# Kernel optimization log

Measured on AMD Instinct MI355X. Metric: run time of the kernel, lower is better.

## Reference

```python
import jax, jax.numpy as jnp
import numpy as np

D_MODEL = 1024
N_HEADS = 16
NUM_EXPERTS = 8
GATE_HIDDEN = 128
B, T = 4, 2048


def setup_inputs() -> dict:
    key = jax.random.key(0)
    ks = jax.random.split(key, 14)
    s = 0.02
    d, e, gh = D_MODEL, NUM_EXPERTS, GATE_HIDDEN
    return {
        "hidden_states": jax.random.normal(ks[0], (B, T, d), jnp.float32),
        # torch Linear weights are [out_features, in_features]
        "Wq": jax.random.normal(ks[1], (e, d, d), jnp.float32) * s,
        "bq": jax.random.normal(ks[2], (e, d), jnp.float32) * s,
        "Wk": jax.random.normal(ks[3], (e, d, d), jnp.float32) * s,
        "bk": jax.random.normal(ks[4], (e, d), jnp.float32) * s,
        "Wv": jax.random.normal(ks[5], (e, d, d), jnp.float32) * s,
        "bv": jax.random.normal(ks[6], (e, d), jnp.float32) * s,
        "Wg1": jax.random.normal(ks[7], (gh, d), jnp.float32) * s,
        "bg1": jax.random.normal(ks[8], (gh,), jnp.float32) * s,
        "Wg2": jax.random.normal(ks[9], (e, gh), jnp.float32) * s,
        "bg2": jax.random.normal(ks[10], (e,), jnp.float32) * s,
        "Wo": jax.random.normal(ks[11], (d, d), jnp.float32) * s,
        "bo": jax.random.normal(ks[12], (d,), jnp.float32) * s,
    }


def reference(hidden_states, Wq, bq, Wk, bk, Wv, bv, Wg1, bg1, Wg2, bg2, Wo, bo):
    Bb, Tt, C = hidden_states.shape
    H = N_HEADS
    Dh = C // H

    # Per-sample gating over mean-pooled sequence
    pooled = hidden_states.mean(axis=1)                        # [B, C]
    gate_h = jax.nn.relu(pooled @ Wg1.T + bg1)                 # [B, 128]
    gw = jax.nn.softmax(gate_h @ Wg2.T + bg2, axis=-1)         # [B, E]

    # Since gating weights are per-batch scalars, sum_e w_e * (x W_e^T + b_e)
    # == x (sum_e w_e W_e)^T + sum_e w_e b_e  — same math, one GEMM per sample.
    def proj(We, be):
        W_eff = jnp.einsum('be,eoi->boi', gw, We)              # [B, C, C]
        b_eff = gw @ be                                        # [B, C]
        y = jnp.einsum('bti,boi->bto', hidden_states, W_eff) + b_eff[:, None, :]
        return y.reshape(Bb, Tt, H, Dh).transpose(0, 2, 1, 3)  # [B, H, T, Dh]

    q = proj(Wq, bq)
    k = proj(Wk, bk)
    v = proj(Wv, bv)

    scores = jnp.einsum('bhtd,bhsd->bhts', q, k) / (Dh ** 0.5)
    attn = jax.nn.softmax(scores, axis=-1)                     # dropout is inference identity
    out = jnp.einsum('bhts,bhsd->bhtd', attn, v)
    out = out.transpose(0, 2, 1, 3).reshape(Bb, Tt, C)
    return out @ Wo.T + bo
```

## Files before the change

### kernel.cpp

```cpp
#include <hip/hip_runtime.h>

#define B_ 4
#define T_ 2048
#define C_ 1024
#define H_ 16
#define DH_ 64
#define E_ 8
#define GH_ 128

typedef unsigned short bf16_t;
typedef __attribute__((ext_vector_type(8))) __bf16 bf16x8;
typedef __attribute__((ext_vector_type(2))) __bf16 bf16x2;
typedef __attribute__((ext_vector_type(4))) float floatx4;
typedef __attribute__((ext_vector_type(16))) float floatx16;

#if __has_builtin(__builtin_amdgcn_exp2f)
#define EXP2F(x) __builtin_amdgcn_exp2f(x)
#else
#define EXP2F(x) exp2f(x)
#endif

__device__ __forceinline__ bf16_t f2bf(float f) {
  unsigned int u = __builtin_bit_cast(unsigned int, f);
  u += 0x7fffu + ((u >> 16) & 1u);
  return (bf16_t)(u >> 16);
}
__device__ __forceinline__ void async16(const void* g, void* l) {
  __builtin_amdgcn_global_load_lds(
      (const __attribute__((address_space(1))) unsigned int*)g,
      (__attribute__((address_space(3))) unsigned int*)l, 16, 0, 0);
}

__global__ void cvt_kernel(const float* __restrict__ src, bf16_t* __restrict__ dst) {
  int i = (blockIdx.x * 256 + threadIdx.x) * 4;
  float4 v = *(const float4*)(src + i);
  bf16_t o4[4] = {f2bf(v.x), f2bf(v.y), f2bf(v.z), f2bf(v.w)};
  *(uint2*)(dst + i) = *(const uint2*)o4;
}

__global__ void pool_kernel(const float* __restrict__ x, float* __restrict__ partial) {
  int bz = blockIdx.x;
  int b = bz >> 4;
  int r0 = (bz & 15) * 128;
  int t = threadIdx.x;
  float a0 = 0.f, a1 = 0.f, a2 = 0.f, a3 = 0.f;
  const float* xb = x + (size_t)b * T_ * C_ + (size_t)r0 * C_;
  for (int r = 0; r < 128; ++r) {
    const float* row = xb + (size_t)r * C_;
    a0 += row[t]; a1 += row[t + 256]; a2 += row[t + 512]; a3 += row[t + 768];
  }
  float* p = partial + (size_t)bz * C_;
  p[t] = a0; p[t + 256] = a1; p[t + 512] = a2; p[t + 768] = a3;
}

__global__ void gate_kernel(const float* __restrict__ partial,
                            const float* __restrict__ Wg1, const float* __restrict__ bg1,
                            const float* __restrict__ Wg2, const float* __restrict__ bg2,
                            const float* __restrict__ bq, const float* __restrict__ bk,
                            const float* __restrict__ bv,
                            float* __restrict__ gw, float* __restrict__ beff) {
  int b = blockIdx.x;
  int t = threadIdx.x;
  __shared__ float spool[C_];
  __shared__ float sh[GH_];
  __shared__ float sgw[E_];
  for (int i = t; i < C_; i += GH_) {
    float s = 0.f;
    for (int j = 0; j < 16; ++j) s += partial[(size_t)(b * 16 + j) * C_ + i];
    spool[i] = s * (1.0f / T_);
  }
  __syncthreads();
  {
    float acc = 0.f;
    const float* wr = Wg1 + (size_t)t * C_;
    for (int i = 0; i < C_; i += 4) {
      float4 w = *(const float4*)(wr + i);
      acc += spool[i] * w.x + spool[i + 1] * w.y + spool[i + 2] * w.z + spool[i + 3] * w.w;
    }
    acc += bg1[t];
    sh[t] = fmaxf(acc, 0.0f);
  }
  __syncthreads();
  if (t < E_) {
    float acc = 0.f;
    const float* wr = Wg2 + t * GH_;
    for (int j = 0; j < GH_; ++j) acc += sh[j] * wr[j];
    sgw[t] = acc + bg2[t];
  }
  __syncthreads();
  if (t == 0) {
    float mx = sgw[0];
    for (int e = 1; e < E_; ++e) mx = fmaxf(mx, sgw[e]);
    float s = 0.f, ex[E_];
    for (int e = 0; e < E_; ++e) { ex[e] = __expf(sgw[e] - mx); s += ex[e]; }
    float inv = 1.0f / s;
    for (int e = 0; e < E_; ++e) { sgw[e] = ex[e] * inv; gw[b * E_ + e] = sgw[e]; }
  }
  __syncthreads();
  for (int o = t; o < C_; o += GH_) {
    float aq = 0.f, ak = 0.f, av = 0.f;
    #pragma unroll
    for (int e = 0; e < E_; ++e) {
      float w = sgw[e];
      aq += w * bq[e * C_ + o];
      ak += w * bk[e * C_ + o];
      av += w * bv[e * C_ + o];
    }
    beff[(0 * B_ + b) * C_ + o] = aq;
    beff[(1 * B_ + b) * C_ + o] = ak;
    beff[(2 * B_ + b) * C_ + o] = av;
  }
}

__global__ void combine_kernel(const float* __restrict__ Wq, const float* __restrict__ Wk,
                               const float* __restrict__ Wv, const float* __restrict__ gw,
                               bf16_t* __restrict__ Weff) {
  int g = blockIdx.x * 256 + threadIdx.x;
  int ig = (g & 127) * 8;
  int o = (g >> 7) & 1023;
  int p = g >> 17;
  const float* W = (p == 0) ? Wq : (p == 1) ? Wk : Wv;
  const float* src = W + (size_t)o * C_ + ig;
  float acc[B_][8];
  #pragma unroll
  for (int b = 0; b < B_; ++b)
    #pragma unroll
    for (int j = 0; j < 8; ++j) acc[b][j] = 0.f;
  #pragma unroll
  for (int e = 0; e < E_; ++e) {
    float4 lo = *(const float4*)(src + (size_t)e * C_ * C_);
    float4 hi = *(const float4*)(src + (size_t)e * C_ * C_ + 4);
    float w8[8] = {lo.x, lo.y, lo.z, lo.w, hi.x, hi.y, hi.z, hi.w};
    #pragma unroll
    for (int b = 0; b < B_; ++b) {
      float wgt = gw[b * E_ + e];
      #pragma unroll
      for (int j = 0; j < 8; ++j) acc[b][j] += wgt * w8[j];
    }
  }
  #pragma unroll
  for (int b = 0; b < B_; ++b) {
    bf16_t out8[8];
    #pragma unroll
    for (int j = 0; j < 8; ++j) out8[j] = f2bf(acc[b][j]);
    *(uint4*)(Weff + ((size_t)p * B_ + b) * C_ * C_ + (size_t)o * C_ + ig) = *(const uint4*)out8;
  }
}

template <int MODE>
__global__ __launch_bounds__(256) void gemm128(const bf16_t* __restrict__ X,
                                               const bf16_t* __restrict__ W,
                                               const float* __restrict__ bias,
                                               bf16_t* __restrict__ Yb,
                                               float* __restrict__ Yf) {
  int n0, m0;
  if (MODE == 0) {
    const int L = blockIdx.x;
    const int wid = (L & 7) * 192 + (L >> 3);
    const int b = wid / 384;
    const int r = wid - b * 384;
    const int p = r >> 7;
    const int r2 = r & 127;
    const int z = p * 4 + b;
    n0 = (r2 & 7) * 128;
    m0 = (r2 >> 3) * 128;
    X += (size_t)b * (T_ * C_);
    W += (size_t)z * (C_ * C_);
    bias += (size_t)z * C_;
    Yb += (size_t)z * (T_ * C_);
  } else {
    const int L = blockIdx.x;
    const int wid = (L & 7) * 64 + (L >> 3);
    n0 = (wid & 7) * 128;
    m0 = (wid >> 3) * 128;
  }

  __shared__ __align__(16) bf16_t As[128][64];
  __shared__ __align__(16) bf16_t Bs[128][64];

  const int tid = threadIdx.x;
  const int wave = tid >> 6;
  const int lane = tid & 63;
  const int quad = lane >> 4;
  const int l16 = lane & 15;
  const int wm = (wave & 1) * 64;
  const int wn = (wave >> 1) * 64;

  floatx4 acc[4][4];
  #pragma unroll
  for (int i = 0; i < 4; ++i)
    #pragma unroll
    for (int j = 0; j < 4; ++j) { floatx4 zz = {0.f, 0.f, 0.f, 0.f}; acc[i][j] = zz; }

  const int ar = tid >> 3;
  const int ac = (tid & 7) * 8;
  const int sc = ((tid & 7) ^ (ar & 7)) * 8;
  const bf16_t* Xp = X + (size_t)(m0 + ar) * C_ + sc;
  const bf16_t* Wp = W + (size_t)(n0 + ar) * C_ + sc;

  const int x7 = l16 & 7;

  for (int k0 = 0; k0 < C_; k0 += 64) {
    __syncthreads();
    #pragma unroll
    for (int s = 0; s < 4; ++s) {
      async16(Xp + (size_t)(s * 32) * C_ + k0, &As[ar + s * 32][ac]);
      async16(Wp + (size_t)(s * 32) * C_ + k0, &Bs[ar + s * 32][ac]);
    }
    __syncthreads();
    #pragma unroll
    for (int kk = 0; kk < 64; kk += 32) {
      const int cofs = (((kk >> 3) + quad) ^ x7) * 8;
      bf16x8 af[4], bfr[4];
      #pragma unroll
      for (int i = 0; i < 4; ++i) {
        af[i] = *(const bf16x8*)(&As[wm + i * 16 + l16][cofs]);
        bfr[i] = *(const bf16x8*)(&Bs[wn + i * 16 + l16][cofs]);
      }
      #pragma unroll
      for (int mi = 0; mi < 4; ++mi)
        #pragma unroll
        for (int ni = 0; ni < 4; ++ni)
          acc[mi][ni] = __builtin_amdgcn_mfma_f32_16x16x32_bf16(af[mi], bfr[ni], acc[mi][ni], 0, 0, 0);
    }
  }

  #pragma unroll
  for (int mi = 0; mi < 4; ++mi) {
    #pragma unroll
    for (int ni = 0; ni < 4; ++ni) {
      const int n = n0 + wn + ni * 16 + l16;
      const float bv = bias[n];
      #pragma unroll
      for (int r = 0; r < 4; ++r) {
        const int m = m0 + wm + mi * 16 + quad * 4 + r;
        float v = acc[mi][ni][r] + bv;
        if (MODE == 0) Yb[((size_t)(n >> 6) * T_ + m) * DH_ + (n & 63)] = f2bf(v);
        else           Yf[(size_t)m * C_ + n] = v;
      }
    }
  }
}

__global__ void vtrans_kernel(const bf16_t* __restrict__ qkv, bf16_t* __restrict__ Vt) {
  const int kt = blockIdx.x;
  const int bh = blockIdx.y;
  const int b = bh >> 4, h = bh & 15;
  const bf16_t* src = qkv + (size_t)(8 + b) * T_ * C_ + (size_t)h * T_ * DH_ + (size_t)kt * 64 * DH_;
  __shared__ __align__(16) bf16_t L[64][64];
  const int t = threadIdx.x;
  const int r = t >> 2;
  const int c = (t & 3) * 16;
  const int sw = r & 48;
  *(uint4*)(&L[r][c ^ sw]) = *(const uint4*)(src + (size_t)r * DH_ + c);
  *(uint4*)(&L[r][(c ^ sw) + 8]) = *(const uint4*)(src + (size_t)r * DH_ + c + 8);
  __syncthreads();
  const int sw2 = c & 48;
  bf16_t tmp[16];
  #pragma unroll
  for (int j = 0; j < 16; ++j) tmp[j] = L[c + j][r ^ sw2];
  bf16_t* dst = Vt + (size_t)bh * DH_ * T_ + (size_t)r * T_ + (size_t)kt * 64 + c;
  *(uint4*)(dst) = *(const uint4*)(tmp);
  *(uint4*)(dst + 8) = *(const uint4*)(tmp + 8);
}

__global__ __launch_bounds__(512, 4) void attn_kernel(const bf16_t* __restrict__ qkv,
                                                      const bf16_t* __restrict__ Vt,
                                                      bf16_t* __restrict__ out) {
  const int bh = blockIdx.x;
  const int qt = blockIdx.y;
  const int b = bh >> 4, h = bh & 15;
  const __bf16* Q = (const __bf16*)(qkv + (size_t)b * T_ * C_ + (size_t)h * T_ * DH_);
  const bf16_t* Kp = qkv + (size_t)(4 + b) * T_ * C_ + (size_t)h * T_ * DH_;
  const bf16_t* Vtb = Vt + (size_t)bh * DH_ * T_;

  __shared__ __align__(16) bf16_t Ks[2][4096];
  __shared__ __align__(16) bf16_t Vs[2][4096];

  const int tid = threadIdx.x;
  const int wave = tid >> 6;
  const int lane = tid & 63;
  const int l31 = lane & 31;
  const int half = lane >> 5;

  const float QSC = 0.125f * 1.44269504f;
  bf16x8 qb[4];
  {
    const __bf16* qrow = Q + (size_t)(qt * 256 + wave * 32 + l31) * DH_;
    #pragma unroll
    for (int kc = 0; kc < 4; ++kc) {
      union { bf16x8 v; __bf16 e[8]; } fr;
      #pragma unroll
      for (int j = 0; j < 8; ++j) fr.e[j] = (__bf16)((float)qrow[kc * 16 + half * 8 + j] * QSC);
      qb[kc] = fr.v;
    }
  }

  int koff[2][4];
  int voff[4][2];
  #pragma unroll
  for (int kb = 0; kb < 2; ++kb)
    #pragma unroll
    for (int kc = 0; kc < 4; ++kc) {
      int r = kb * 32 + l31;
      koff[kb][kc] = (r * 8 + ((kc * 2 + half) ^ (r & 7))) * 8;
    }
  #pragma unroll
  for (int c = 0; c < 4; ++c)
    #pragma unroll
    for (int db = 0; db < 2; ++db) {
      int r = db * 32 + l31;
      voff[c][db] = (r * 8 + ((c * 2 + half) ^ (r & 7))) * 8;
    }

  floatx16 oacc[2];
  #pragma unroll
  for (int db = 0; db < 2; ++db)
    #pragma unroll
    for (int i = 0; i < 16; ++i) oacc[db][i] = 0.f;
  float lrun = 0.f;

  const int srow = tid >> 3;
  const int schk = (tid & 7) ^ (srow & 7);
  const bf16_t* kg = Kp + (size_t)srow * DH_ + schk * 8;
  const bf16_t* vg = Vtb + (size_t)srow * T_ + schk * 8;

#define STAGE(BUF) do {                                   \
    async16(kg, &Ks[BUF][tid * 8]);                       \
    async16(vg, &Vs[BUF][tid * 8]);                       \
    kg += 64 * DH_;                                       \
    vg += 64;                                             \
  } while (0)

#define WAITV(N) asm volatile("s_waitcnt vmcnt(" #N ")" ::: "memory")
#define BAR() __builtin_amdgcn_s_barrier()

#define COMPUTE(CUR) do {                                                            \
    _Pragma("unroll")                                                                \
    for (int kb = 0; kb < 2; ++kb) {                                                 \
      floatx16 s_;                                                                   \
      _Pragma("unroll")                                                              \
      for (int i = 0; i < 16; ++i) s_[i] = 0.f;                                      \
      __builtin_amdgcn_s_setprio(1);                                                 \
      _Pragma("unroll")                                                              \
      for (int kc = 0; kc < 4; ++kc) {                                               \
        bf16x8 ka = *(const bf16x8*)(&Ks[CUR][koff[kb][kc]]);                        \
        s_ = __builtin_amdgcn_mfma_f32_32x32x16_bf16(ka, qb[kc], s_, 0, 0, 0);       \
      }                                                                              \
      __builtin_amdgcn_s_setprio(0);                                                 \
      _Pragma("unroll")                                                              \
      for (int cl = 0; cl < 2; ++cl) {                                               \
        float e0 = EXP2F(s_[cl * 8 + 0]);                                            \
        float e1 = EXP2F(s_[cl * 8 + 1]);                                            \
        float e2 = EXP2F(s_[cl * 8 + 2]);                                            \
        float e3 = EXP2F(s_[cl * 8 + 3]);                                            \
        float e4 = EXP2F(s_[cl * 8 + 4]);                                            \
        float e5 = EXP2F(s_[cl * 8 + 5]);                                            \
        float e6 = EXP2F(s_[cl * 8 + 6]);                                            \
        float e7 = EXP2F(s_[cl * 8 + 7]);                                            \
        lrun += ((e0 + e1) + (e2 + e3)) + ((e4 + e5) + (e6 + e7));                   \
        bf16x2 w01 = {(__bf16)e0, (__bf16)e1};                                       \
        bf16x2 w23 = {(__bf16)e2, (__bf16)e3};                                       \
        bf16x2 w45 = {(__bf16)e4, (__bf16)e5};                                       \
        bf16x2 w67 = {(__bf16)e6, (__bf16)e7};                                       \
        unsigned int ua = __builtin_bit_cast(unsigned int, w01);                     \
        unsigned int ub = __builtin_bit_cast(unsigned int, w23);                     \
        unsigned int uc = __builtin_bit_cast(unsigned int, w45);                     \
        unsigned int ud = __builtin_bit_cast(unsigned int, w67);                     \
        asm("v_permlane32_swap_b32 %0, %1" : "+v"(ua), "+v"(uc));                    \
        asm("v_permlane32_swap_b32 %0, %1" : "+v"(ub), "+v"(ud));                    \
        union { unsigned int u[4]; bf16x8 v; } pf;                                   \
        pf.u[0] = ua; pf.u[1] = ub; pf.u[2] = uc; pf.u[3] = ud;                      \
        __builtin_amdgcn_s_setprio(1);                                               \
        _Pragma("unroll")                                                            \
        for (int db = 0; db < 2; ++db) {                                             \
          bf16x8 vb = *(const bf16x8*)(&Vs[CUR][voff[kb * 2 + cl][db]]);             \
          oacc[db] = __builtin_amdgcn_mfma_f32_32x32x16_bf16(pf.v, vb, oacc[db], 0, 0, 0); \
        }                                                                            \
        __builtin_amdgcn_s_setprio(0);                                               \
      }                                                                              \
    }                                                                                \
  } while (0)

  STAGE(0);
  #pragma unroll 1
  for (int kt = 0; kt < 30; kt += 2) {
    STAGE(1);
    WAITV(2);
    BAR();
    COMPUTE(0);
    BAR();
    STAGE(0);
    WAITV(2);
    BAR();
    COMPUTE(1);
    BAR();
  }
  STAGE(1);
  WAITV(2);
  BAR();
  COMPUTE(0);
  BAR();
  WAITV(0);
  BAR();
  COMPUTE(1);

#undef STAGE
#undef WAITV
#undef BAR
#undef COMPUTE

  lrun += __shfl_xor(lrun, 32);
  float linv = 1.0f / lrun;
  #pragma unroll
  for (int reg = 0; reg < 16; ++reg) {
    int mr = (reg & 3) + 8 * (reg >> 2) + 4 * half;
    float li = __shfl(linv, (lane & 32) | mr);
    int m = qt * 256 + wave * 32 + mr;
    #pragma unroll
    for (int db = 0; db < 2; ++db) {
      out[(size_t)b * T_ * C_ + (size_t)m * C_ + h * DH_ + db * 32 + l31] =
          f2bf(oacc[db][reg] * li);
    }
  }
}

extern "C" void kernel_launch(void* const* d_in, const int* in_sizes, int n_in,
                              void* d_out, int out_size, void* d_ws, size_t ws_size,
                              hipStream_t stream) {
  (void)in_sizes; (void)n_in; (void)out_size; (void)ws_size;
  const float* x   = (const float*)d_in[0];
  const float* Wq  = (const float*)d_in[1];
  const float* bq  = (const float*)d_in[2];
  const float* Wk  = (const float*)d_in[3];
  const float* bk  = (const float*)d_in[4];
  const float* Wv  = (const float*)d_in[5];
  const float* bv  = (const float*)d_in[6];
  const float* Wg1 = (const float*)d_in[7];
  const float* bg1 = (const float*)d_in[8];
  const float* Wg2 = (const float*)d_in[9];
  const float* bg2 = (const float*)d_in[10];
  const float* Wo  = (const float*)d_in[11];
  const float* bo  = (const float*)d_in[12];

  char* ws = (char*)d_ws;
  size_t off = 0;
  auto alloc = [&](size_t bytes) -> void* {
    void* p = ws + off;
    off += (bytes + 255) & ~(size_t)255;
    return p;
  };
  float* partial = (float*)alloc((size_t)B_ * 16 * C_ * 4);
  float* gw      = (float*)alloc((size_t)B_ * E_ * 4);
  float* beff    = (float*)alloc((size_t)3 * B_ * C_ * 4);
  bf16_t* xbf    = (bf16_t*)alloc((size_t)B_ * T_ * C_ * 2);
  bf16_t* Wobf   = (bf16_t*)alloc((size_t)C_ * C_ * 2);
  bf16_t* Weff   = (bf16_t*)alloc((size_t)3 * B_ * C_ * C_ * 2);
  bf16_t* qkv    = (bf16_t*)alloc((size_t)3 * B_ * T_ * C_ * 2);
  bf16_t* attn   = (bf16_t*)alloc((size_t)B_ * T_ * C_ * 2);
  bf16_t* Vt = xbf;

  pool_kernel<<<dim3(B_ * 16), 256, 0, stream>>>(x, partial);
  gate_kernel<<<dim3(B_), GH_, 0, stream>>>(partial, Wg1, bg1, Wg2, bg2,
                                            bq, bk, bv, gw, beff);
  combine_kernel<<<dim3(3 * C_ * (C_ / 8) / 256), 256, 0, stream>>>(Wq, Wk, Wv, gw, Weff);
  cvt_kernel<<<dim3((B_ * T_ * C_) / 1024), 256, 0, stream>>>(x, xbf);
  cvt_kernel<<<dim3((C_ * C_) / 1024), 256, 0, stream>>>(Wo, Wobf);
  gemm128<0><<<dim3(12 * (T_ / 128) * (C_ / 128)), 256, 0, stream>>>(xbf, Weff, beff, qkv, nullptr);
  vtrans_kernel<<<dim3(T_ / 64, B_ * H_), 256, 0, stream>>>(qkv, Vt);
  attn_kernel<<<dim3(B_ * H_, T_ / 256), 512, 0, stream>>>(qkv, Vt, attn);
  gemm128<1><<<dim3(((B_ * T_) / 128) * (C_ / 128)), 256, 0, stream>>>(attn, Wobf, bo, nullptr, (float*)d_out);
}
```

Measured before the change: 411.1 us.

## Fuse x bf16 conversion into pooling; shrink attention blocks to 256 threads

The pooling kernel now also writes the bf16 copy of the hidden states. This removes the separate conversion pass and a second full read of x. It uses 256 blocks of 32 rows with float4 loads, and the gate kernel sums 64 partials instead of 16. The attention kernel moves from 512-thread blocks covering 256 queries to 256-thread blocks covering 128 queries, doubling the grid. Each thread now issues two async loads each for K and V per stage, so the wait counts are adjusted and the V offsets reuse the K offset table.

```diff
diff --git a/kernel.cpp b/kernel.cpp
--- a/kernel.cpp
+++ b/kernel.cpp
@@ -38,19 +38,22 @@
   *(uint2*)(dst + i) = *(const uint2*)o4;
 }
 
-__global__ void pool_kernel(const float* __restrict__ x, float* __restrict__ partial) {
-  int bz = blockIdx.x;
-  int b = bz >> 4;
-  int r0 = (bz & 15) * 128;
-  int t = threadIdx.x;
-  float a0 = 0.f, a1 = 0.f, a2 = 0.f, a3 = 0.f;
-  const float* xb = x + (size_t)b * T_ * C_ + (size_t)r0 * C_;
-  for (int r = 0; r < 128; ++r) {
-    const float* row = xb + (size_t)r * C_;
-    a0 += row[t]; a1 += row[t + 256]; a2 += row[t + 512]; a3 += row[t + 768];
-  }
-  float* p = partial + (size_t)bz * C_;
-  p[t] = a0; p[t + 256] = a1; p[t + 512] = a2; p[t + 768] = a3;
+__global__ void pool_kernel(const float* __restrict__ x, float* __restrict__ partial,
+                            bf16_t* __restrict__ xbf) {
+  const int bz = blockIdx.x;
+  const int b = bz >> 6;
+  const int r0 = (bz & 63) * 32;
+  const int t = threadIdx.x;
+  float4 acc = {0.f, 0.f, 0.f, 0.f};
+  const float* xb = x + (size_t)b * T_ * C_ + (size_t)r0 * C_ + t * 4;
+  bf16_t* ob = xbf + (size_t)b * T_ * C_ + (size_t)r0 * C_ + t * 4;
+  for (int r = 0; r < 32; ++r) {
+    float4 v = *(const float4*)(xb + (size_t)r * C_);
+    acc.x += v.x; acc.y += v.y; acc.z += v.z; acc.w += v.w;
+    bf16_t o4[4] = {f2bf(v.x), f2bf(v.y), f2bf(v.z), f2bf(v.w)};
+    *(uint2*)(ob + (size_t)r * C_) = *(const uint2*)o4;
+  }
+  *(float4*)(partial + (size_t)bz * C_ + t * 4) = acc;
 }
 
 __global__ void gate_kernel(const float* __restrict__ partial,
@@ -66,7 +69,7 @@
   __shared__ float sgw[E_];
   for (int i = t; i < C_; i += GH_) {
     float s = 0.f;
-    for (int j = 0; j < 16; ++j) s += partial[(size_t)(b * 16 + j) * C_ + i];
+    for (int j = 0; j < 64; ++j) s += partial[(size_t)(b * 64 + j) * C_ + i];
     spool[i] = s * (1.0f / T_);
   }
   __syncthreads();
@@ -264,7 +267,7 @@
   *(uint4*)(dst + 8) = *(const uint4*)(tmp + 8);
 }
 
-__global__ __launch_bounds__(512, 4) void attn_kernel(const bf16_t* __restrict__ qkv,
+__global__ __launch_bounds__(256, 4) void attn_kernel(const bf16_t* __restrict__ qkv,
                                                       const bf16_t* __restrict__ Vt,
                                                       bf16_t* __restrict__ out) {
   const int bh = blockIdx.x;
@@ -286,7 +289,7 @@
   const float QSC = 0.125f * 1.44269504f;
   bf16x8 qb[4];
   {
-    const __bf16* qrow = Q + (size_t)(qt * 256 + wave * 32 + l31) * DH_;
+    const __bf16* qrow = Q + (size_t)(qt * 128 + wave * 32 + l31) * DH_;
     #pragma unroll
     for (int kc = 0; kc < 4; ++kc) {
       union { bf16x8 v; __bf16 e[8]; } fr;
@@ -297,20 +300,12 @@
   }
 
   int koff[2][4];
-  int voff[4][2];
   #pragma unroll
   for (int kb = 0; kb < 2; ++kb)
     #pragma unroll
     for (int kc = 0; kc < 4; ++kc) {
       int r = kb * 32 + l31;
       koff[kb][kc] = (r * 8 + ((kc * 2 + half) ^ (r & 7))) * 8;
-    }
-  #pragma unroll
-  for (int c = 0; c < 4; ++c)
-    #pragma unroll
-    for (int db = 0; db < 2; ++db) {
-      int r = db * 32 + l31;
-      voff[c][db] = (r * 8 + ((c * 2 + half) ^ (r & 7))) * 8;
     }
 
   floatx16 oacc[2];
@@ -325,11 +320,13 @@
   const bf16_t* kg = Kp + (size_t)srow * DH_ + schk * 8;
   const bf16_t* vg = Vtb + (size_t)srow * T_ + schk * 8;
 
-#define STAGE(BUF) do {                                   \
-    async16(kg, &Ks[BUF][tid * 8]);                       \
-    async16(vg, &Vs[BUF][tid * 8]);                       \
-    kg += 64 * DH_;                                       \
-    vg += 64;                                             \
+#define STAGE(BUF) do {                                           \
+    async16(kg, &Ks[BUF][tid * 8]);                               \
+    async16(kg + 32 * DH_, &Ks[BUF][2048 + tid * 8]);             \
+    async16(vg, &Vs[BUF][tid * 8]);                               \
+    async16(vg + (size_t)32 * T_, &Vs[BUF][2048 + tid * 8]);      \
+    kg += 64 * DH_;                                               \
+    vg += 64;                                                     \
   } while (0)
 
 #define WAITV(N) asm volatile("s_waitcnt vmcnt(" #N ")" ::: "memory")
@@ -374,7 +371,7 @@
         __builtin_amdgcn_s_setprio(1);                                               \
         _Pragma("unroll")                                                            \
         for (int db = 0; db < 2; ++db) {                                             \
-          bf16x8 vb = *(const bf16x8*)(&Vs[CUR][voff[kb * 2 + cl][db]]);             \
+          bf16x8 vb = *(const bf16x8*)(&Vs[CUR][koff[db][kb * 2 + cl]]);             \
           oacc[db] = __builtin_amdgcn_mfma_f32_32x32x16_bf16(pf.v, vb, oacc[db], 0, 0, 0); \
         }                                                                            \
         __builtin_amdgcn_s_setprio(0);                                               \
@@ -386,18 +383,18 @@
   #pragma unroll 1
   for (int kt = 0; kt < 30; kt += 2) {
     STAGE(1);
-    WAITV(2);
+    WAITV(4);
     BAR();
     COMPUTE(0);
     BAR();
     STAGE(0);
-    WAITV(2);
+    WAITV(4);
     BAR();
     COMPUTE(1);
     BAR();
   }
   STAGE(1);
-  WAITV(2);
+  WAITV(4);
   BAR();
   COMPUTE(0);
   BAR();
@@ -416,7 +413,7 @@
   for (int reg = 0; reg < 16; ++reg) {
     int mr = (reg & 3) + 8 * (reg >> 2) + 4 * half;
     float li = __shfl(linv, (lane & 32) | mr);
-    int m = qt * 256 + wave * 32 + mr;
+    int m = qt * 128 + wave * 32 + mr;
     #pragma unroll
     for (int db = 0; db < 2; ++db) {
       out[(size_t)b * T_ * C_ + (size_t)m * C_ + h * DH_ + db * 32 + l31] =
@@ -450,7 +447,7 @@
     off += (bytes + 255) & ~(size_t)255;
     return p;
   };
-  float* partial = (float*)alloc((size_t)B_ * 16 * C_ * 4);
+  float* partial = (float*)alloc((size_t)B_ * 64 * C_ * 4);
   float* gw      = (float*)alloc((size_t)B_ * E_ * 4);
   float* beff    = (float*)alloc((size_t)3 * B_ * C_ * 4);
   bf16_t* xbf    = (bf16_t*)alloc((size_t)B_ * T_ * C_ * 2);
@@ -460,14 +457,13 @@
   bf16_t* attn   = (bf16_t*)alloc((size_t)B_ * T_ * C_ * 2);
   bf16_t* Vt = xbf;
 
-  pool_kernel<<<dim3(B_ * 16), 256, 0, stream>>>(x, partial);
+  pool_kernel<<<dim3(B_ * 64), 256, 0, stream>>>(x, partial, xbf);
   gate_kernel<<<dim3(B_), GH_, 0, stream>>>(partial, Wg1, bg1, Wg2, bg2,
                                             bq, bk, bv, gw, beff);
   combine_kernel<<<dim3(3 * C_ * (C_ / 8) / 256), 256, 0, stream>>>(Wq, Wk, Wv, gw, Weff);
-  cvt_kernel<<<dim3((B_ * T_ * C_) / 1024), 256, 0, stream>>>(x, xbf);
   cvt_kernel<<<dim3((C_ * C_) / 1024), 256, 0, stream>>>(Wo, Wobf);
   gemm128<0><<<dim3(12 * (T_ / 128) * (C_ / 128)), 256, 0, stream>>>(xbf, Weff, beff, qkv, nullptr);
   vtrans_kernel<<<dim3(T_ / 64, B_ * H_), 256, 0, stream>>>(qkv, Vt);
-  attn_kernel<<<dim3(B_ * H_, T_ / 256), 512, 0, stream>>>(qkv, Vt, attn);
+  attn_kernel<<<dim3(B_ * H_, T_ / 128), 256, 0, stream>>>(qkv, Vt, attn);
   gemm128<1><<<dim3(((B_ * T_) / 128) * (C_ / 128)), 256, 0, stream>>>(attn, Wobf, bo, nullptr, (float*)d_out);
 }
```

Result: no change. 409.0 us (-0.5%).

## Fuse x bf16 conversion into pooling, bias mixing and V transpose into QKV GEMM

Applied to the files above, without the earlier changes.

The pooling kernel now also writes the bf16 copy of the input, so the separate conversion pass over x is gone and x is read once. The effective bias mixing moves from the gate kernel into the QKV GEMM epilogue, which forms it from the gating weights. The V projection is written directly in transposed [d][t] layout through an LDS-staged, swizzled epilogue, which removes the separate vtrans kernel and its extra read and write of V. In exchange the GEMM epilogue does more work and the pooling uses four times as many partial sums.

```diff
diff --git a/kernel.cpp b/kernel.cpp
--- a/kernel.cpp
+++ b/kernel.cpp
@@ -38,27 +38,28 @@
   *(uint2*)(dst + i) = *(const uint2*)o4;
 }
 
-__global__ void pool_kernel(const float* __restrict__ x, float* __restrict__ partial) {
-  int bz = blockIdx.x;
-  int b = bz >> 4;
-  int r0 = (bz & 15) * 128;
-  int t = threadIdx.x;
-  float a0 = 0.f, a1 = 0.f, a2 = 0.f, a3 = 0.f;
-  const float* xb = x + (size_t)b * T_ * C_ + (size_t)r0 * C_;
-  for (int r = 0; r < 128; ++r) {
-    const float* row = xb + (size_t)r * C_;
-    a0 += row[t]; a1 += row[t + 256]; a2 += row[t + 512]; a3 += row[t + 768];
-  }
-  float* p = partial + (size_t)bz * C_;
-  p[t] = a0; p[t + 256] = a1; p[t + 512] = a2; p[t + 768] = a3;
+__global__ void pool_kernel(const float* __restrict__ x, float* __restrict__ partial,
+                            bf16_t* __restrict__ xbf) {
+  const int bz = blockIdx.x;
+  const int b = bz >> 6;
+  const int r0 = (bz & 63) * 32;
+  const int t = threadIdx.x;
+  float4 acc = {0.f, 0.f, 0.f, 0.f};
+  const float* xb = x + (size_t)b * T_ * C_ + (size_t)r0 * C_ + t * 4;
+  bf16_t* ob = xbf + (size_t)b * T_ * C_ + (size_t)r0 * C_ + t * 4;
+  for (int r = 0; r < 32; ++r) {
+    float4 v = *(const float4*)(xb + (size_t)r * C_);
+    acc.x += v.x; acc.y += v.y; acc.z += v.z; acc.w += v.w;
+    bf16_t o4[4] = {f2bf(v.x), f2bf(v.y), f2bf(v.z), f2bf(v.w)};
+    *(uint2*)(ob + (size_t)r * C_) = *(const uint2*)o4;
+  }
+  *(float4*)(partial + (size_t)bz * C_ + t * 4) = acc;
 }
 
 __global__ void gate_kernel(const float* __restrict__ partial,
                             const float* __restrict__ Wg1, const float* __restrict__ bg1,
                             const float* __restrict__ Wg2, const float* __restrict__ bg2,
-                            const float* __restrict__ bq, const float* __restrict__ bk,
-                            const float* __restrict__ bv,
-                            float* __restrict__ gw, float* __restrict__ beff) {
+                            float* __restrict__ gw) {
   int b = blockIdx.x;
   int t = threadIdx.x;
   __shared__ float spool[C_];
@@ -66,7 +67,7 @@
   __shared__ float sgw[E_];
   for (int i = t; i < C_; i += GH_) {
     float s = 0.f;
-    for (int j = 0; j < 16; ++j) s += partial[(size_t)(b * 16 + j) * C_ + i];
+    for (int j = 0; j < 64; ++j) s += partial[(size_t)(b * 64 + j) * C_ + i];
     spool[i] = s * (1.0f / T_);
   }
   __syncthreads();
@@ -94,21 +95,7 @@
     float s = 0.f, ex[E_];
     for (int e = 0; e < E_; ++e) { ex[e] = __expf(sgw[e] - mx); s += ex[e]; }
     float inv = 1.0f / s;
-    for (int e = 0; e < E_; ++e) { sgw[e] = ex[e] * inv; gw[b * E_ + e] = sgw[e]; }
-  }
-  __syncthreads();
-  for (int o = t; o < C_; o += GH_) {
-    float aq = 0.f, ak = 0.f, av = 0.f;
-    #pragma unroll
-    for (int e = 0; e < E_; ++e) {
-      float w = sgw[e];
-      aq += w * bq[e * C_ + o];
-      ak += w * bk[e * C_ + o];
-      av += w * bv[e * C_ + o];
-    }
-    beff[(0 * B_ + b) * C_ + o] = aq;
-    beff[(1 * B_ + b) * C_ + o] = ak;
-    beff[(2 * B_ + b) * C_ + o] = av;
+    for (int e = 0; e < E_; ++e) gw[b * E_ + e] = ex[e] * inv;
   }
 }
 
@@ -151,9 +138,15 @@
 __global__ __launch_bounds__(256) void gemm128(const bf16_t* __restrict__ X,
                                                const bf16_t* __restrict__ W,
                                                const float* __restrict__ bias,
+                                               const float* __restrict__ bq,
+                                               const float* __restrict__ bk,
+                                               const float* __restrict__ bv,
+                                               const float* __restrict__ gw,
                                                bf16_t* __restrict__ Yb,
                                                float* __restrict__ Yf) {
   int n0, m0;
+  int pp = 0, bb = 0;
+  const float* bsrc = nullptr;
   if (MODE == 0) {
     const int L = blockIdx.x;
     const int wid = (L & 7) * 192 + (L >> 3);
@@ -166,8 +159,9 @@
     m0 = (r2 >> 3) * 128;
     X += (size_t)b * (T_ * C_);
     W += (size_t)z * (C_ * C_);
-    bias += (size_t)z * C_;
     Yb += (size_t)z * (T_ * C_);
+    pp = p; bb = b;
+    bsrc = (p == 0) ? bq : (p == 1) ? bk : bv;
   } else {
     const int L = blockIdx.x;
     const int wid = (L & 7) * 64 + (L >> 3);
@@ -175,8 +169,9 @@
     m0 = (wid >> 3) * 128;
   }
 
-  __shared__ __align__(16) bf16_t As[128][64];
-  __shared__ __align__(16) bf16_t Bs[128][64];
+  __shared__ __align__(16) bf16_t smem[2][128][64];
+  bf16_t (*As)[64] = smem[0];
+  bf16_t (*Bs)[64] = smem[1];
 
   const int tid = threadIdx.x;
   const int wave = tid >> 6;
@@ -186,6 +181,12 @@
   const int wm = (wave & 1) * 64;
   const int wn = (wave >> 1) * 64;
 
+  float gwv[E_];
+  if (MODE == 0) {
+    #pragma unroll
+    for (int e = 0; e < E_; ++e) gwv[e] = gw[bb * E_ + e];
+  }
+
   floatx4 acc[4][4];
   #pragma unroll
   for (int i = 0; i < 4; ++i)
@@ -225,16 +226,63 @@
     }
   }
 
+  float be_[4];
+  #pragma unroll
+  for (int ni = 0; ni < 4; ++ni) {
+    const int n = n0 + wn + ni * 16 + l16;
+    if (MODE == 0) {
+      float s = 0.f;
+      #pragma unroll
+      for (int e = 0; e < E_; ++e) s += gwv[e] * bsrc[(size_t)e * C_ + n];
+      be_[ni] = s;
+    } else {
+      be_[ni] = bias[n];
+    }
+  }
+
+  if (MODE == 0 && pp == 2) {
+    __syncthreads();
+    bf16_t* Ls = &smem[0][0][0];
+    #pragma unroll
+    for (int ni = 0; ni < 4; ++ni) {
+      const int n = wn + ni * 16 + l16;
+      #pragma unroll
+      for (int mi = 0; mi < 4; ++mi) {
+        const int mb = wm + mi * 16 + quad * 4;
+        bf16_t o4[4];
+        #pragma unroll
+        for (int r = 0; r < 4; ++r) o4[r] = f2bf(acc[mi][ni][r] + be_[ni]);
+        const int c = mb >> 3;
+        const int csw = (c & 8) | ((c ^ n) & 7);
+        *(uint2*)((char*)(Ls + (size_t)n * 128) + csw * 16 + (mb & 7) * 2) =
+            *(const uint2*)o4;
+      }
+    }
+    __syncthreads();
+    const int n = tid >> 1;
+    const int mh = (tid & 1) * 64;
+    const int head = (n0 + n) >> 6;
+    const int d = (n0 + n) & 63;
+    bf16_t* dst = Yb + (size_t)head * (DH_ * T_) + (size_t)d * T_ + m0 + mh;
+    #pragma unroll
+    for (int j = 0; j < 8; ++j) {
+      const int c = (mh >> 3) + j;
+      const int csw = (c & 8) | ((c ^ n) & 7);
+      *(uint4*)(dst + j * 8) =
+          *(const uint4*)((const char*)(Ls + (size_t)n * 128) + csw * 16);
+    }
+    return;
+  }
+
   #pragma unroll
   for (int mi = 0; mi < 4; ++mi) {
     #pragma unroll
     for (int ni = 0; ni < 4; ++ni) {
       const int n = n0 + wn + ni * 16 + l16;
-      const float bv = bias[n];
       #pragma unroll
       for (int r = 0; r < 4; ++r) {
         const int m = m0 + wm + mi * 16 + quad * 4 + r;
-        float v = acc[mi][ni][r] + bv;
+        float v = acc[mi][ni][r] + be_[ni];
         if (MODE == 0) Yb[((size_t)(n >> 6) * T_ + m) * DH_ + (n & 63)] = f2bf(v);
         else           Yf[(size_t)m * C_ + n] = v;
       }
@@ -242,37 +290,14 @@
   }
 }
 
-__global__ void vtrans_kernel(const bf16_t* __restrict__ qkv, bf16_t* __restrict__ Vt) {
-  const int kt = blockIdx.x;
-  const int bh = blockIdx.y;
-  const int b = bh >> 4, h = bh & 15;
-  const bf16_t* src = qkv + (size_t)(8 + b) * T_ * C_ + (size_t)h * T_ * DH_ + (size_t)kt * 64 * DH_;
-  __shared__ __align__(16) bf16_t L[64][64];
-  const int t = threadIdx.x;
-  const int r = t >> 2;
-  const int c = (t & 3) * 16;
-  const int sw = r & 48;
-  *(uint4*)(&L[r][c ^ sw]) = *(const uint4*)(src + (size_t)r * DH_ + c);
-  *(uint4*)(&L[r][(c ^ sw) + 8]) = *(const uint4*)(src + (size_t)r * DH_ + c + 8);
-  __syncthreads();
-  const int sw2 = c & 48;
-  bf16_t tmp[16];
-  #pragma unroll
-  for (int j = 0; j < 16; ++j) tmp[j] = L[c + j][r ^ sw2];
-  bf16_t* dst = Vt + (size_t)bh * DH_ * T_ + (size_t)r * T_ + (size_t)kt * 64 + c;
-  *(uint4*)(dst) = *(const uint4*)(tmp);
-  *(uint4*)(dst + 8) = *(const uint4*)(tmp + 8);
-}
-
 __global__ __launch_bounds__(512, 4) void attn_kernel(const bf16_t* __restrict__ qkv,
-                                                      const bf16_t* __restrict__ Vt,
                                                       bf16_t* __restrict__ out) {
   const int bh = blockIdx.x;
   const int qt = blockIdx.y;
   const int b = bh >> 4, h = bh & 15;
   const __bf16* Q = (const __bf16*)(qkv + (size_t)b * T_ * C_ + (size_t)h * T_ * DH_);
   const bf16_t* Kp = qkv + (size_t)(4 + b) * T_ * C_ + (size_t)h * T_ * DH_;
-  const bf16_t* Vtb = Vt + (size_t)bh * DH_ * T_;
+  const bf16_t* Vtb = qkv + (size_t)(8 + b) * T_ * C_ + (size_t)h * DH_ * T_;
 
   __shared__ __align__(16) bf16_t Ks[2][4096];
   __shared__ __align__(16) bf16_t Vs[2][4096];
@@ -450,24 +475,21 @@
     off += (bytes + 255) & ~(size_t)255;
     return p;
   };
-  float* partial = (float*)alloc((size_t)B_ * 16 * C_ * 4);
+  float* partial = (float*)alloc((size_t)B_ * 64 * C_ * 4);
   float* gw      = (float*)alloc((size_t)B_ * E_ * 4);
-  float* beff    = (float*)alloc((size_t)3 * B_ * C_ * 4);
   bf16_t* xbf    = (bf16_t*)alloc((size_t)B_ * T_ * C_ * 2);
   bf16_t* Wobf   = (bf16_t*)alloc((size_t)C_ * C_ * 2);
   bf16_t* Weff   = (bf16_t*)alloc((size_t)3 * B_ * C_ * C_ * 2);
   bf16_t* qkv    = (bf16_t*)alloc((size_t)3 * B_ * T_ * C_ * 2);
   bf16_t* attn   = (bf16_t*)alloc((size_t)B_ * T_ * C_ * 2);
-  bf16_t* Vt = xbf;
-
-  pool_kernel<<<dim3(B_ * 16), 256, 0, stream>>>(x, partial);
-  gate_kernel<<<dim3(B_), GH_, 0, stream>>>(partial, Wg1, bg1, Wg2, bg2,
-                                            bq, bk, bv, gw, beff);
+
+  pool_kernel<<<dim3(B_ * 64), 256, 0, stream>>>(x, partial, xbf);
+  gate_kernel<<<dim3(B_), GH_, 0, stream>>>(partial, Wg1, bg1, Wg2, bg2, gw);
   combine_kernel<<<dim3(3 * C_ * (C_ / 8) / 256), 256, 0, stream>>>(Wq, Wk, Wv, gw, Weff);
-  cvt_kernel<<<dim3((B_ * T_ * C_) / 1024), 256, 0, stream>>>(x, xbf);
   cvt_kernel<<<dim3((C_ * C_) / 1024), 256, 0, stream>>>(Wo, Wobf);
-  gemm128<0><<<dim3(12 * (T_ / 128) * (C_ / 128)), 256, 0, stream>>>(xbf, Weff, beff, qkv, nullptr);
-  vtrans_kernel<<<dim3(T_ / 64, B_ * H_), 256, 0, stream>>>(qkv, Vt);
-  attn_kernel<<<dim3(B_ * H_, T_ / 256), 512, 0, stream>>>(qkv, Vt, attn);
-  gemm128<1><<<dim3(((B_ * T_) / 128) * (C_ / 128)), 256, 0, stream>>>(attn, Wobf, bo, nullptr, (float*)d_out);
-}
+  gemm128<0><<<dim3(12 * (T_ / 128) * (C_ / 128)), 256, 0, stream>>>(
+      xbf, Weff, nullptr, bq, bk, bv, gw, qkv, nullptr);
+  attn_kernel<<<dim3(B_ * H_, T_ / 256), 512, 0, stream>>>(qkv, attn);
+  gemm128<1><<<dim3(((B_ * T_) / 128) * (C_ / 128)), 256, 0, stream>>>(
+      attn, Wobf, bo, nullptr, nullptr, nullptr, nullptr, nullptr, (float*)d_out);
+}
```

After: 401.3 us. 2.4% less time.
